# Kernel optimization log

Measured on AMD Instinct MI355X. Metric: run time of the kernel, lower is better.

The kernel has to match this reference:

```python
import jax, jax.numpy as jnp
import numpy as np

N_GRAPH = 10000
IN_DIM = 256
HID = 256
N_NODES = 16
FEAT_DIM = 64
N_EDGES = 5
TAU = 0.01


def _gat(x, src, dst, W, al, ar, R, b, H, D, N):
    # DGL GATConv: fc -> per-head attention logits -> edge softmax over dst -> aggregate, residual fc, bias
    h = (x @ W).reshape(N, H, D)                      # [N,H,D]
    el = jnp.sum(h * al[None], -1)                    # [N,H]
    er = jnp.sum(h * ar[None], -1)                    # [N,H]
    e = jax.nn.leaky_relu(el[src] + er[dst], 0.2)     # [E,H]
    m = jax.ops.segment_max(e, dst, num_segments=N)
    ex = jnp.exp(e - m[dst])
    s = jax.ops.segment_sum(ex, dst, num_segments=N)
    alpha = ex / s[dst]                               # [E,H]
    out = jax.ops.segment_sum(alpha[:, :, None] * h[src], dst, num_segments=N)  # [N,H,D]
    out = out + (x @ R).reshape(N, H, D) + b.reshape(1, H, D)
    return out.reshape(N, H * D)


def _masked_softmax(vec, mask, eps=1e-8):
    m = mask.astype(vec.dtype)
    _vec = vec * m - 10000.0 * (1.0 - m)
    vmax = jnp.max(_vec, axis=-1, keepdims=True)
    exps = jnp.exp((vec - vmax) * m) * m
    return exps / (jnp.sum(exps, -1, keepdims=True) + eps)


def _sample_edges(probs, target_idx):
    n, T = probs.shape
    mask = jnp.arange(T) == target_idx                # [T] bool, one-hot of target
    edges = [jnp.full((n,), target_idx, dtype=jnp.int32)]
    key = jax.random.key(42)
    for i in range(N_EDGES - 1):
        p = _masked_softmax(probs, jnp.logical_not(mask))
        idx = jax.random.categorical(jax.random.fold_in(key, i),
                                     jnp.log(jnp.maximum(p, 1e-30)), axis=-1)  # [n]
        mask = jnp.logical_or(jax.nn.one_hot(idx, T, dtype=bool), mask)
        edges.append(idx.astype(jnp.int32))
    return jnp.stack(edges, axis=-1)                  # [n, N_EDGES]


def _forward(feat, W1a, al1a, ar1a, R1a, b1a, W1e, al1e, ar1e, R1e, b1e,
             W2a, al2a, ar2a, R2a, b2a, W2e, al2e, ar2e, R2e, b2e,
             Wt, bt, Wo, bo, src, dst, target_idx):
    N = feat.shape[0]
    tf = jax.nn.leaky_relu(feat[target_idx] @ Wt + bt, 0.01)            # [2*HID]
    a = _gat(feat, src, dst, W1a, al1a, ar1a, R1a, b1a, 4, HID // 4, N)  # [N,HID]
    e = _gat(feat, src, dst, W1e, al1e, ar1e, R1e, b1e, 4, HID // 4, N)  # [N,HID]
    a2 = jax.nn.leaky_relu(jnp.concatenate([a, e], -1) + tf, 0.01)       # [N,2*HID]
    e2 = jax.nn.leaky_relu(jnp.concatenate([e, a], -1) + tf, 0.01)
    a3 = _gat(a2, src, dst, W2a, al2a, ar2a, R2a, b2a, 4, N_NODES * FEAT_DIM // 4, N)  # [N, n_nodes*feat_dim]
    e3 = _gat(e2, src, dst, W2e, al2e, ar2e, R2e, b2e, 1, N_NODES, N)                  # [N, n_nodes]
    attr = a3.reshape(N, N_NODES, FEAT_DIM).mean(0)                     # [n_nodes, feat_dim]
    node_attr = jax.nn.leaky_relu(attr, 0.01) @ Wo + bo                 # [n_nodes, input_dim]
    probs = jax.nn.softmax(e3.T, axis=-1)                               # [n_nodes, N]
    return node_attr, probs


def setup_inputs() -> dict:
    key = jax.random.key(0)
    ks = jax.random.split(key, 32)
    N, IN, H = N_GRAPH, IN_DIM, 4
    E0 = 80000
    feat = jax.random.normal(ks[0], (N, IN), jnp.float32)
    loop = jnp.arange(N, dtype=jnp.int32)
    src = jnp.concatenate([jax.random.randint(ks[1], (E0,), 0, N, jnp.int32), loop])
    dst = jnp.concatenate([jax.random.randint(ks[2], (E0,), 0, N, jnp.int32), loop])

    def p(k, shape, fan):
        return jax.random.normal(k, shape, jnp.float32) * (1.0 / np.sqrt(fan))

    D1 = HID // 4
    D2a = N_NODES * FEAT_DIM // 4
    O2a = N_NODES * FEAT_DIM
    inp = dict(feat=feat, src=src, dst=dst, target_idx=7)
    # layer-1 attr / edge GATs
    inp.update(W1a=p(ks[3], (IN, HID), IN), al1a=p(ks[4], (H, D1), D1), ar1a=p(ks[5], (H, D1), D1),
               R1a=p(ks[6], (IN, HID), IN), b1a=p(ks[7], (HID,), HID))
    inp.update(W1e=p(ks[8], (IN, HID), IN), al1e=p(ks[9], (H, D1), D1), ar1e=p(ks[10], (H, D1), D1),
               R1e=p(ks[11], (IN, HID), IN), b1e=p(ks[12], (HID,), HID))
    # layer-2 attr GAT (4 heads) and edge GAT (1 head)
    inp.update(W2a=p(ks[13], (2 * HID, O2a), 2 * HID), al2a=p(ks[14], (H, D2a), D2a), ar2a=p(ks[15], (H, D2a), D2a),
               R2a=p(ks[16], (2 * HID, O2a), 2 * HID), b2a=p(ks[17], (O2a,), O2a))
    inp.update(W2e=p(ks[18], (2 * HID, N_NODES), 2 * HID), al2e=p(ks[19], (1, N_NODES), N_NODES),
               ar2e=p(ks[20], (1, N_NODES), N_NODES), R2e=p(ks[21], (2 * HID, N_NODES), 2 * HID),
               b2e=p(ks[22], (N_NODES,), N_NODES))
    # target feat layer and attr output layer
    inp.update(Wt=p(ks[23], (IN, 2 * HID), IN), bt=p(ks[24], (2 * HID,), 2 * HID),
               Wo=p(ks[25], (FEAT_DIM, IN), FEAT_DIM), bo=p(ks[26], (IN,), IN))
    return inp


def reference(feat, W1a, al1a, ar1a, R1a, b1a, W1e, al1e, ar1e, R1e, b1e,
              W2a, al2a, ar2a, R2a, b2a, W2e, al2e, ar2e, R2e, b2e,
              Wt, bt, Wo, bo, src, dst, target_idx):
    node_attr, probs = _forward(feat, W1a, al1a, ar1a, R1a, b1a, W1e, al1e, ar1e, R1e, b1e,
                                W2a, al2a, ar2a, R2a, b2a, W2e, al2e, ar2e, R2e, b2e,
                                Wt, bt, Wo, bo, src, dst, target_idx)
    node_edges = _sample_edges(probs, target_idx)
    # (node_attr, attr_sample_weights, node_edges, normalized_edge_sample_weights)
    return node_attr, node_attr, node_edges, probs
```

## Files before the change

kernel.cpp:

```cpp
#include <hip/hip_runtime.h>
#include <hip/hip_bf16.h>

#define NGR 10000
typedef unsigned int u32;
typedef __attribute__((ext_vector_type(8))) short short8;
typedef __attribute__((ext_vector_type(4))) float f32x4;

__device__ __forceinline__ void threefry(u32 k0, u32 k1, u32 c0, u32 c1, u32& o0, u32& o1) {
    u32 ks2 = k0 ^ k1 ^ 0x1BD11BDAu;
    u32 x0 = c0 + k0, x1 = c1 + k1;
#define TF_R(r) { x0 += x1; x1 = (x1 << r) | (x1 >> (32 - r)); x1 ^= x0; }
    TF_R(13) TF_R(15) TF_R(26) TF_R(6)
    x0 += k1; x1 += ks2 + 1u;
    TF_R(17) TF_R(29) TF_R(16) TF_R(24)
    x0 += ks2; x1 += k0 + 2u;
    TF_R(13) TF_R(15) TF_R(26) TF_R(6)
    x0 += k0; x1 += k1 + 3u;
    TF_R(17) TF_R(29) TF_R(16) TF_R(24)
    x0 += k1; x1 += ks2 + 4u;
    TF_R(13) TF_R(15) TF_R(26) TF_R(6)
    x0 += ks2; x1 += k0 + 5u;
#undef TF_R
    o0 = x0; o1 = x1;
}

__global__ void k_deg(const int* __restrict__ dst, int* __restrict__ deg, int E) {
    int i = blockIdx.x * blockDim.x + threadIdx.x;
    if (i < E) atomicAdd(&deg[dst[i]], 1);
}
__global__ void k_scan(const int* __restrict__ deg, int* __restrict__ rowptr, int n) {
    __shared__ int sums[256];
    __shared__ int excl[257];
    const int T = 256;
    int t = threadIdx.x;
    int per = (n + T - 1) / T;
    int lo = t * per, hi = min(lo + per, n);
    int s = 0;
    for (int i = lo; i < hi; ++i) s += deg[i];
    sums[t] = s;
    __syncthreads();
    if (t == 0) { int run = 0; for (int i = 0; i < T; ++i) { excl[i] = run; run += sums[i]; } excl[T] = run; }
    __syncthreads();
    int run = excl[t];
    for (int i = lo; i < hi; ++i) { rowptr[i] = run; run += deg[i]; }
    if (t == 0) rowptr[n] = excl[T];
}
__global__ void k_scatter(const int* __restrict__ dst, const int* __restrict__ rowptr,
                          int* __restrict__ cursor, int* __restrict__ colidx, int E) {
    int i = blockIdx.x * blockDim.x + threadIdx.x;
    if (i >= E) return;
    int d = dst[i];
    int pos = atomicAdd(&cursor[d], 1);
    colidx[rowptr[d] + pos] = i;
}

#define TINYF 1.17549435e-38f
__global__ __launch_bounds__(256) void k_prep(
    const float* __restrict__ feat, const int* __restrict__ tptr,
    const float* __restrict__ Wt, const float* __restrict__ bt,
    const float* __restrict__ W1a, const float* __restrict__ W1e,
    const float* __restrict__ R1a, const float* __restrict__ R1e,
    const float* __restrict__ b1a, const float* __restrict__ b1e,
    const float* __restrict__ W2a, const float* __restrict__ al2a, const float* __restrict__ ar2a,
    unsigned short* __restrict__ feathi, unsigned short* __restrict__ featlo,
    unsigned short* __restrict__ WThi, unsigned short* __restrict__ WTlo,
    float* __restrict__ tf, float* __restrict__ gum, float* __restrict__ wal,
    float* __restrict__ packb, float* __restrict__ zreg)
{
    __shared__ float sh[32 * 33];
    int b = blockIdx.x, tid = threadIdx.x;
    if (b < 2500) {
        int idx = b * 256 + tid;
        float4 v = ((const float4*)feat)[idx];
        ushort4 h, l;
        __hip_bfloat16 bb; float r;
        bb = __float2bfloat16(v.x); h.x = *(unsigned short*)&bb; r = v.x - __bfloat162float(bb);
        bb = __float2bfloat16(r);   l.x = *(unsigned short*)&bb;
        bb = __float2bfloat16(v.y); h.y = *(unsigned short*)&bb; r = v.y - __bfloat162float(bb);
        bb = __float2bfloat16(r);   l.y = *(unsigned short*)&bb;
        bb = __float2bfloat16(v.z); h.z = *(unsigned short*)&bb; r = v.z - __bfloat162float(bb);
        bb = __float2bfloat16(r);   l.z = *(unsigned short*)&bb;
        bb = __float2bfloat16(v.w); h.w = *(unsigned short*)&bb; r = v.w - __bfloat162float(bb);
        bb = __float2bfloat16(r);   l.w = *(unsigned short*)&bb;
        ((ushort4*)feathi)[idx] = h;
        ((ushort4*)featlo)[idx] = l;
        return;
    }
    b -= 2500;
    if (b < 256) {
        int bx = b >> 3, by = b & 7;
        int tx = tid & 31, ty = tid >> 5;
#pragma unroll
        for (int i = ty; i < 32; i += 8) {
            int k = by * 32 + i, c = bx * 32 + tx;
            float v;
            if (c < 256) v = W1a[k * 256 + c];
            else if (c < 512) v = W1e[k * 256 + c - 256];
            else if (c < 768) v = R1a[k * 256 + c - 512];
            else v = R1e[k * 256 + c - 768];
            sh[i * 33 + tx] = v;
        }
        __syncthreads();
#pragma unroll
        for (int i = ty; i < 32; i += 8) {
            float x = sh[tx * 33 + i];
            __hip_bfloat16 bh = __float2bfloat16(x);
            float r = x - __bfloat162float(bh);
            __hip_bfloat16 bl = __float2bfloat16(r);
            WThi[(size_t)(bx * 32 + i) * 256 + by * 32 + tx] = *(unsigned short*)&bh;
            WTlo[(size_t)(bx * 32 + i) * 256 + by * 32 + tx] = *(unsigned short*)&bl;
        }
        return;
    }
    b -= 256;
    if (b < 8) {
        float* frow = sh;
        float* red = sh + 256;
        int t = *tptr;
        frow[tid] = feat[t * 256 + tid];
        __syncthreads();
        int j = b * 64 + (tid & 63);
        int ks = (tid >> 6) * 64;
        float s = 0.f;
#pragma unroll 16
        for (int k = ks; k < ks + 64; ++k) s = fmaf(frow[k], Wt[(size_t)k * 512 + j], s);
        red[tid] = s;
        __syncthreads();
        if (tid < 64) {
            float v = red[tid] + red[tid + 64] + red[tid + 128] + red[tid + 192] + bt[j];
            tf[j] = v >= 0.f ? v : 0.01f * v;
        }
        return;
    }
    b -= 8;
    if (b < 2500) {
        int idx = b * 256 + tid;
        int it = idx / (16 * NGR);
        int f = idx - it * (16 * NGR);
        u32 fk0, fk1, o0, o1;
        threefry(0u, 42u, 0u, (u32)it, fk0, fk1);
        threefry(fk0, fk1, 0u, (u32)f, o0, o1);
        u32 bits = o0 ^ o1;
        float fl = __uint_as_float((bits >> 9) | 0x3F800000u) - 1.0f;
        float u = fmaxf(TINYF, fl + TINYF);
        gum[idx] = -logf(-logf(u));
        return;
    }
    b -= 2500;
    if (b < 16) {
        int o = b * 256 + tid;
        int k = o >> 3, q = o & 7, sel = q >> 2, hh = q & 3;
        const float* av = (sel ? ar2a : al2a) + hh * 256;
        const float* wr = W2a + (size_t)k * 1024 + hh * 256;
        float s = 0.f;
        for (int d = 0; d < 256; ++d) s = fmaf(wr[d], av[d], s);
        wal[k * 8 + q] = s;
        return;
    }
    b -= 16;
    if (b < 235) {
        int idx = b * 256 + tid;
        if (idx < NGR * 6) zreg[idx] = 0.f;
        return;
    }
    b -= 235;
    {
        int c = b * 256 + tid;
        packb[c] = (c < 512) ? 0.f : ((c < 768) ? b1a[c - 512] : b1e[c - 768]);
    }
}

__global__ __launch_bounds__(256) void gemm_bf16x3(
    const unsigned short* __restrict__ Ahi, const unsigned short* __restrict__ Alo,
    const unsigned short* __restrict__ Bhi, const unsigned short* __restrict__ Blo,
    float* __restrict__ C, const float* __restrict__ bias, int M)
{
    constexpr int K = 256;
    __shared__ unsigned short AsH[2][128 * 32];
    __shared__ unsigned short AsL[2][128 * 32];
    __shared__ unsigned short BsH[2][128 * 32];
    __shared__ unsigned short BsL[2][128 * 32];
    const int tid = threadIdx.x;
    const int lane = tid & 63;
    const int w = tid >> 6, wr = w >> 1, wc = w & 1;
    const int bm = blockIdx.y * 128, bn = blockIdx.x * 128;
    const int fr = lane & 15, fq = lane >> 4;
    const int srow = tid >> 2;
    const int sbyte = (tid & 3) * 16;
    f32x4 acc[4][4] = {};

    auto stage = [&](int b, int k0) {
        const char* pA[2] = {(const char*)Ahi, (const char*)Alo};
        const char* pB[2] = {(const char*)Bhi, (const char*)Blo};
        char* dA[2] = {(char*)AsH[b], (char*)AsL[b]};
        char* dB[2] = {(char*)BsH[b], (char*)BsL[b]};
#pragma unroll
        for (int q = 0; q < 2; ++q) {
            const char* ga0 = pA[q] + ((size_t)(bm + srow) * K + k0) * 2 + sbyte;
            const char* ga1 = pA[q] + ((size_t)(bm + 64 + srow) * K + k0) * 2 + sbyte;
            const char* gb0 = pB[q] + ((size_t)(bn + srow) * K + k0) * 2 + sbyte;
            const char* gb1 = pB[q] + ((size_t)(bn + 64 + srow) * K + k0) * 2 + sbyte;
            __builtin_amdgcn_global_load_lds((const __attribute__((address_space(1))) void*)ga0,
                (__attribute__((address_space(3))) void*)(dA[q] + tid * 16), 16, 0, 0);
            __builtin_amdgcn_global_load_lds((const __attribute__((address_space(1))) void*)ga1,
                (__attribute__((address_space(3))) void*)(dA[q] + 4096 + tid * 16), 16, 0, 0);
            __builtin_amdgcn_global_load_lds((const __attribute__((address_space(1))) void*)gb0,
                (__attribute__((address_space(3))) void*)(dB[q] + tid * 16), 16, 0, 0);
            __builtin_amdgcn_global_load_lds((const __attribute__((address_space(1))) void*)gb1,
                (__attribute__((address_space(3))) void*)(dB[q] + 4096 + tid * 16), 16, 0, 0);
        }
    };

    stage(0, 0);
    __syncthreads();
    int buf = 0;
    for (int t = 0; t < 8; ++t) {
        if (t < 7) stage(buf ^ 1, (t + 1) * 32);
        const char* ah = (const char*)AsH[buf];
        const char* al = (const char*)AsL[buf];
        const char* bh = (const char*)BsH[buf];
        const char* bl = (const char*)BsL[buf];
        short8 afh[4], afl[4], bfh[4], bfl[4];
#pragma unroll
        for (int m = 0; m < 4; ++m) {
            int o = (wr * 64 + m * 16 + fr) * 64 + fq * 16;
            afh[m] = *(const short8*)(ah + o);
            afl[m] = *(const short8*)(al + o);
        }
#pragma unroll
        for (int n = 0; n < 4; ++n) {
            int o = (wc * 64 + n * 16 + fr) * 64 + fq * 16;
            bfh[n] = *(const short8*)(bh + o);
            bfl[n] = *(const short8*)(bl + o);
        }
#pragma unroll
        for (int m = 0; m < 4; ++m)
#pragma unroll
            for (int n = 0; n < 4; ++n) {
                acc[m][n] = __builtin_amdgcn_mfma_f32_16x16x32_bf16(afl[m], bfh[n], acc[m][n], 0, 0, 0);
                acc[m][n] = __builtin_amdgcn_mfma_f32_16x16x32_bf16(afh[m], bfl[n], acc[m][n], 0, 0, 0);
                acc[m][n] = __builtin_amdgcn_mfma_f32_16x16x32_bf16(afh[m], bfh[n], acc[m][n], 0, 0, 0);
            }
        __syncthreads();
        buf ^= 1;
    }
#pragma unroll
    for (int m = 0; m < 4; ++m) {
#pragma unroll
        for (int i = 0; i < 4; ++i) {
            int row = bm + wr * 64 + m * 16 + fq * 4 + i;
            if (row >= M) continue;
#pragma unroll
            for (int n = 0; n < 4; ++n) {
                int col = bn + wc * 64 + n * 16 + fr;
                C[(size_t)row * 1024 + col] = acc[m][n][i] + bias[col];
            }
        }
    }
}

__global__ void k_el_er_l1(const float* __restrict__ h,
                           const float* __restrict__ al1a, const float* __restrict__ ar1a,
                           const float* __restrict__ al1e, const float* __restrict__ ar1e,
                           float* __restrict__ el, float* __restrict__ er, int N)
{
    int idx = blockIdx.x * blockDim.x + threadIdx.x;
    if (idx >= N * 8) return;
    int n = idx >> 3, sub = idx & 7;
    int role = sub >> 2, hh = sub & 3;
    const float* hp = h + (size_t)n * 1024 + role * 256 + hh * 64;
    const float* alp = (role ? al1e : al1a) + hh * 64;
    const float* arp = (role ? ar1e : ar1a) + hh * 64;
    float sl = 0.f, sr = 0.f;
    for (int d = 0; d < 64; d += 4) {
        float4 v = *(const float4*)(hp + d);
        float4 a4 = *(const float4*)(alp + d);
        float4 r4 = *(const float4*)(arp + d);
        sl = fmaf(v.x, a4.x, sl); sl = fmaf(v.y, a4.y, sl); sl = fmaf(v.z, a4.z, sl); sl = fmaf(v.w, a4.w, sl);
        sr = fmaf(v.x, r4.x, sr); sr = fmaf(v.y, r4.y, sr); sr = fmaf(v.z, r4.z, sr); sr = fmaf(v.w, r4.w, sr);
    }
    el[n * 8 + sub] = sl;
    er[n * 8 + sub] = sr;
}

__global__ void k_softmax_csr(const float* __restrict__ el, const float* __restrict__ er,
                              const int* __restrict__ rowptr, const int* __restrict__ colidx,
                              const int* __restrict__ src,
                              float* __restrict__ ee, int H, int hshift, int total)
{
    int idx = blockIdx.x * blockDim.x + threadIdx.x;
    if (idx >= total) return;
    int n = idx >> hshift, hh = idx & (H - 1);
    float ern = er[n * H + hh];
    int i0 = rowptr[n], i1 = rowptr[n + 1];
    float mx = -INFINITY;
    for (int i = i0; i < i1; ++i) {
        float v = el[src[colidx[i]] * H + hh] + ern;
        v = v >= 0.f ? v : 0.2f * v;
        mx = fmaxf(mx, v);
    }
    float s = 0.f;
    for (int i = i0; i < i1; ++i) {
        int e = colidx[i];
        float v = el[src[e] * H + hh] + ern;
        v = v >= 0.f ? v : 0.2f * v;
        float ex = expf(v - mx);
        ee[(size_t)e * H + hh] = ex;
        s += ex;
    }
    for (int i = i0; i < i1; ++i) {
        int e = colidx[i];
        ee[(size_t)e * H + hh] /= s;
    }
}

__global__ void k_agg_csr4(const float* __restrict__ alpha,
                           const int* __restrict__ rowptr, const int* __restrict__ colidx,
                           const int* __restrict__ src,
                           const float* __restrict__ h, int ldh4, int hoff4,
                           float* __restrict__ out, int ldo4, int ooff4,
                           int H, int dshift4, int hdshift4, int total)
{
    int idx = blockIdx.x * blockDim.x + threadIdx.x;
    if (idx >= total) return;
    int n = idx >> hdshift4, c4 = idx & ((1 << hdshift4) - 1);
    int hh = c4 >> dshift4;
    const float4* h4 = (const float4*)h;
    float4* out4 = (float4*)out;
    float4 acc = out4[(size_t)n * ldo4 + ooff4 + c4];
    int i1 = rowptr[n + 1];
    for (int i = rowptr[n]; i < i1; ++i) {
        int e = colidx[i];
        float a = alpha[(size_t)e * H + hh];
        float4 hv = h4[(size_t)src[e] * ldh4 + hoff4 + c4];
        acc.x = fmaf(a, hv.x, acc.x); acc.y = fmaf(a, hv.y, acc.y);
        acc.z = fmaf(a, hv.z, acc.z); acc.w = fmaf(a, hv.w, acc.w);
    }
    out4[(size_t)n * ldo4 + ooff4 + c4] = acc;
}

__global__ void k_a2e2(const float* __restrict__ h1o1, const float* __restrict__ tf,
                       float* __restrict__ B)
{
    int idx = blockIdx.x * blockDim.x + threadIdx.x;
    if (idx >= NGR * 256) return;
    int n = idx >> 8, c4 = idx & 255;
    int c = c4 << 2;
    const float* o = h1o1 + (size_t)n * 1024 + 512;
    float4 x;
    if (c < 512) x = *(const float4*)(o + c);
    else { int cc = c - 512; x = *(const float4*)(o + ((cc < 256) ? cc + 256 : cc - 256)); }
    float4 t4 = *(const float4*)(tf + (c & 511));
    x.x += t4.x; x.y += t4.y; x.z += t4.z; x.w += t4.w;
    x.x = x.x >= 0.f ? x.x : 0.01f * x.x;
    x.y = x.y >= 0.f ? x.y : 0.01f * x.y;
    x.z = x.z >= 0.f ? x.z : 0.01f * x.z;
    x.w = x.w >= 0.f ? x.w : 0.01f * x.w;
    *(float4*)(B + (size_t)n * 1024 + c) = x;
}

__global__ __launch_bounds__(256) void k_node_linear(
    const float* __restrict__ a2e2,
    const float* __restrict__ We, const float* __restrict__ Re, const float* __restrict__ be,
    const float* __restrict__ wal,
    const float* __restrict__ al2e, const float* __restrict__ ar2e,
    float* __restrict__ h2e, float* __restrict__ e3,
    float* __restrict__ el2e, float* __restrict__ er2e,
    float* __restrict__ el2a, float* __restrict__ er2a)
{
    __shared__ float As[8 * 1024];
    __shared__ float red[2048];
    __shared__ float hl[8][16];
    int tid = threadIdx.x;
    int m0 = blockIdx.x * 8;
    for (int i = tid; i < 8 * 256; i += 256) {
        int row = i >> 8, c4 = (i & 255) << 2;
        *(float4*)(As + row * 1024 + c4) = *(const float4*)(a2e2 + (size_t)(m0 + row) * 1024 + c4);
    }
    __syncthreads();
    {
        int j = tid & 31, ks = tid >> 5;
        const float* B = (j < 16) ? We : Re;
        int jj = j & 15;
        float acc[8] = {};
        int k0 = ks * 64;
        for (int kk = 0; kk < 64; kk += 4) {
            int k = k0 + kk;
            float b0 = B[(k + 0) * 16 + jj];
            float b1 = B[(k + 1) * 16 + jj];
            float b2 = B[(k + 2) * 16 + jj];
            float b3 = B[(k + 3) * 16 + jj];
#pragma unroll
            for (int r = 0; r < 8; ++r) {
                float4 a = *(const float4*)(As + r * 1024 + 512 + k);
                acc[r] = fmaf(a.x, b0, acc[r]);
                acc[r] = fmaf(a.y, b1, acc[r]);
                acc[r] = fmaf(a.z, b2, acc[r]);
                acc[r] = fmaf(a.w, b3, acc[r]);
            }
        }
#pragma unroll
        for (int r = 0; r < 8; ++r) red[(r * 32 + j) * 8 + ks] = acc[r];
    }
    __syncthreads();
    {
        int r = tid >> 5, jo = tid & 31;
        const float* rp = red + (r * 32 + jo) * 8;
        float acc = ((rp[0] + rp[1]) + (rp[2] + rp[3])) + ((rp[4] + rp[5]) + (rp[6] + rp[7]));
        int m = m0 + r, jj = jo & 15;
        if (jo < 16) { h2e[(size_t)m * 16 + jj] = acc; hl[r][jj] = acc; }
        else         e3[(size_t)m * 16 + jj] = acc + be[jj];
    }
    __syncthreads();
    {
        int q = tid & 7, ks2 = tid >> 3;
        float acc[8] = {};
        int k0 = ks2 * 16;
        for (int kk = 0; kk < 16; ++kk) {
            int k = k0 + kk;
            float b = wal[k * 8 + q];
#pragma unroll
            for (int r = 0; r < 8; ++r)
                acc[r] = fmaf(As[r * 1024 + k], b, acc[r]);
        }
#pragma unroll
        for (int r = 0; r < 8; ++r) red[(r * 8 + q) * 32 + ks2] = acc[r];
    }
    __syncthreads();
    if (tid < 64) {
        const float* rp = red + tid * 32;
        float acc = 0.f;
#pragma unroll
        for (int g = 0; g < 32; ++g) acc += rp[g];
        int r = tid >> 3, q = tid & 7;
        int m = m0 + r;
        if (q < 4) el2a[m * 4 + q] = acc;
        else       er2a[m * 4 + (q - 4)] = acc;
    }
    if (tid >= 64 && tid < 72) {
        int rr = tid - 64;
        float sl = 0.f, sr = 0.f;
        const float* hp = hl[rr];
        for (int d = 0; d < 16; ++d) { float v = hp[d]; sl = fmaf(v, al2e[d], sl); sr = fmaf(v, ar2e[d], sr); }
        el2e[m0 + rr] = sl;
        er2e[m0 + rr] = sr;
    }
}

__global__ void k_sm2a_wa(const float* __restrict__ el, const float* __restrict__ er,
                          const int* __restrict__ rowptr, const int* __restrict__ colidx,
                          const int* __restrict__ src,
                          float* __restrict__ walpha, int total)
{
    int idx = blockIdx.x * blockDim.x + threadIdx.x;
    if (idx >= total) return;
    int n = idx >> 2, hh = idx & 3;
    float ern = er[n * 4 + hh];
    int i0 = rowptr[n], i1 = rowptr[n + 1];
    float mx = -INFINITY;
    for (int i = i0; i < i1; ++i) {
        float v = el[src[colidx[i]] * 4 + hh] + ern;
        v = v >= 0.f ? v : 0.2f * v;
        mx = fmaxf(mx, v);
    }
    float s = 0.f;
    for (int i = i0; i < i1; ++i) {
        float v = el[src[colidx[i]] * 4 + hh] + ern;
        v = v >= 0.f ? v : 0.2f * v;
        s += expf(v - mx);
    }
    for (int i = i0; i < i1; ++i) {
        int e = colidx[i];
        int sn = src[e];
        float v = el[sn * 4 + hh] + ern;
        v = v >= 0.f ? v : 0.2f * v;
        float alpha = expf(v - mx) / s;
        atomicAdd(&walpha[sn * 4 + hh], alpha);
    }
}

__global__ void k_smagg2e(const float* __restrict__ el, const float* __restrict__ er,
                          const int* __restrict__ rowptr, const int* __restrict__ colidx,
                          const int* __restrict__ src,
                          const float* __restrict__ h2e, float* __restrict__ e3, int N)
{
    int n = blockIdx.x * blockDim.x + threadIdx.x;
    if (n >= N) return;
    float ern = er[n];
    int i0 = rowptr[n], i1 = rowptr[n + 1];
    float mx = -INFINITY;
    for (int i = i0; i < i1; ++i) {
        float v = el[src[colidx[i]]] + ern;
        v = v >= 0.f ? v : 0.2f * v;
        mx = fmaxf(mx, v);
    }
    float s = 0.f;
    for (int i = i0; i < i1; ++i) {
        float v = el[src[colidx[i]]] + ern;
        v = v >= 0.f ? v : 0.2f * v;
        s += expf(v - mx);
    }
    float4* e34 = (float4*)(e3 + (size_t)n * 16);
    float4 a0 = e34[0], a1 = e34[1], a2 = e34[2], a3 = e34[3];
    for (int i = i0; i < i1; ++i) {
        int e = colidx[i];
        int sn = src[e];
        float v = el[sn] + ern;
        v = v >= 0.f ? v : 0.2f * v;
        float al = expf(v - mx) / s;
        const float4* hp = (const float4*)(h2e + (size_t)sn * 16);
        float4 h0 = hp[0], h1 = hp[1], h2 = hp[2], h3 = hp[3];
        a0.x = fmaf(al, h0.x, a0.x); a0.y = fmaf(al, h0.y, a0.y); a0.z = fmaf(al, h0.z, a0.z); a0.w = fmaf(al, h0.w, a0.w);
        a1.x = fmaf(al, h1.x, a1.x); a1.y = fmaf(al, h1.y, a1.y); a1.z = fmaf(al, h1.z, a1.z); a1.w = fmaf(al, h1.w, a1.w);
        a2.x = fmaf(al, h2.x, a2.x); a2.y = fmaf(al, h2.y, a2.y); a2.z = fmaf(al, h2.z, a2.z); a2.w = fmaf(al, h2.w, a2.w);
        a3.x = fmaf(al, h3.x, a3.x); a3.y = fmaf(al, h3.y, a3.y); a3.z = fmaf(al, h3.z, a3.z); a3.w = fmaf(al, h3.w, a3.w);
    }
    e34[0] = a0; e34[1] = a1; e34[2] = a2; e34[3] = a3;
}

__global__ __launch_bounds__(256) void k_pwa(const float* __restrict__ a2e2,
                                             const float* __restrict__ walpha,
                                             float* __restrict__ pwa)
{
    int b = blockIdx.x, t = threadIdx.x;
    float acc[5][2] = {};
    int n0 = b * 80, n1 = min(n0 + 80, NGR);
    for (int n = n0; n < n1; ++n) {
        const float* row = a2e2 + (size_t)n * 1024;
        const float* wa = walpha + n * 4;
        float w0 = wa[0], w1 = wa[1], w2 = wa[2], w3 = wa[3];
        float x0 = row[t], x1 = row[t + 256];
        acc[0][0] = fmaf(w0, x0, acc[0][0]); acc[0][1] = fmaf(w0, x1, acc[0][1]);
        acc[1][0] = fmaf(w1, x0, acc[1][0]); acc[1][1] = fmaf(w1, x1, acc[1][1]);
        acc[2][0] = fmaf(w2, x0, acc[2][0]); acc[2][1] = fmaf(w2, x1, acc[2][1]);
        acc[3][0] = fmaf(w3, x0, acc[3][0]); acc[3][1] = fmaf(w3, x1, acc[3][1]);
        acc[4][0] += x0; acc[4][1] += x1;
    }
#pragma unroll
    for (int q = 0; q < 5; ++q) {
        pwa[(size_t)b * 2560 + q * 512 + t] = acc[q][0];
        pwa[(size_t)b * 2560 + q * 512 + t + 256] = acc[q][1];
    }
}
__global__ void k_pwa_fin(const float* __restrict__ pwa, float* __restrict__ waw)
{
    int idx = blockIdx.x * blockDim.x + threadIdx.x;
    if (idx >= 2560) return;
    float s = 0.f;
    for (int b = 0; b < 125; ++b) s += pwa[(size_t)b * 2560 + idx];
    waw[idx] = s;
}

__global__ __launch_bounds__(256) void k_gemv3(const float* __restrict__ waw,
                                               const float* __restrict__ W2a, const float* __restrict__ R2a,
                                               const float* __restrict__ b2a,
                                               float* __restrict__ attrL)
{
    __shared__ float red[256];
    int b = blockIdx.x, t = threadIdx.x;
    int c = b * 16 + (t & 15);
    int hh = (b * 16) >> 8;
    int ks = (t >> 4) * 32;
    const float* wh = waw + hh * 512;
    const float* w4 = waw + 4 * 512;
    float s = 0.f;
#pragma unroll 8
    for (int k = ks; k < ks + 32; ++k) {
        s = fmaf(wh[k], W2a[(size_t)k * 1024 + c], s);
        s = fmaf(w4[k], R2a[(size_t)k * 1024 + c], s);
    }
    red[t] = s;
    __syncthreads();
    if (t < 16) {
        float v = 0.f;
#pragma unroll
        for (int g = 0; g < 16; ++g) v += red[t + g * 16];
        v = v / (float)NGR + b2a[b * 16 + t];
        attrL[b * 16 + t] = v >= 0.f ? v : 0.01f * v;
    }
}

__global__ __launch_bounds__(256) void k_nattr2(const float* __restrict__ attrL,
                                                const float* __restrict__ Wo, const float* __restrict__ bo,
                                                float* __restrict__ out)
{
    __shared__ float al[64];
    int i = blockIdx.x, t = threadIdx.x;
    if (t < 64) al[t] = attrL[i * 64 + t];
    __syncthreads();
    float acc = 0.f;
#pragma unroll 8
    for (int d = 0; d < 64; ++d) acc = fmaf(al[d], Wo[d * 256 + t], acc);
    acc += bo[t];
    out[i * 256 + t] = acc;
    out[4096 + i * 256 + t] = acc;
}

__global__ __launch_bounds__(256) void k_e3stats(const float* __restrict__ e3,
                                                 float* __restrict__ pm, float* __restrict__ ps)
{
    __shared__ float lds[4000];
    __shared__ float redm[16][16];
    __shared__ float reds[16][16];
    __shared__ float cm[16];
    int b = blockIdx.x, tid = threadIdx.x;
    int base = b * 250 * 16;
    for (int i = tid; i < 4000; i += 256) lds[i] = e3[base + i];
    __syncthreads();
    int c = tid & 15, g = tid >> 4;
    float mx = -INFINITY;
    for (int q = g; q < 250; q += 16) mx = fmaxf(mx, lds[q * 16 + c]);
    redm[c][g] = mx;
    __syncthreads();
    if (tid < 16) {
        float m = redm[tid][0];
        for (int q = 1; q < 16; ++q) m = fmaxf(m, redm[tid][q]);
        cm[tid] = m;
    }
    __syncthreads();
    float mb = cm[c];
    float s = 0.f;
    for (int q = g; q < 250; q += 16) s += expf(lds[q * 16 + c] - mb);
    reds[c][g] = s;
    __syncthreads();
    if (tid < 16) {
        float ss = 0.f;
        for (int q = 0; q < 16; ++q) ss += reds[tid][q];
        pm[b * 16 + tid] = cm[tid];
        ps[b * 16 + tid] = ss;
    }
}
__global__ void k_e3fin(const float* __restrict__ pm, const float* __restrict__ ps,
                        float* __restrict__ mx16, float* __restrict__ ss16)
{
    int c = threadIdx.x;
    if (c >= 16) return;
    float M = -INFINITY;
    for (int b = 0; b < 40; ++b) M = fmaxf(M, pm[b * 16 + c]);
    float S = 0.f;
    for (int b = 0; b < 40; ++b) S += ps[b * 16 + c] * expf(pm[b * 16 + c] - M);
    mx16[c] = M;
    ss16[c] = S;
}

__global__ __launch_bounds__(256) void k_top5(const float* __restrict__ e3, const float* __restrict__ gum,
                                              const float* __restrict__ mx16, const float* __restrict__ ss16,
                                              float* __restrict__ probs,
                                              float* __restrict__ t5v, int* __restrict__ t5i)
{
    __shared__ float wv[4];
    __shared__ int wi[4];
    int chunk = blockIdx.x, y = blockIdx.y;
    int it = y >> 4, r = y & 15;
    int tid = threadIdx.x, lane = tid & 63, wid = tid >> 6;
    float mxr = mx16[r], ssr = ss16[r];
    const float* g = gum + (size_t)y * NGR;
    int jb = chunk * 1250;
    float sv[5]; int si[5];
#pragma unroll
    for (int q = 0; q < 5; ++q) {
        int o = q * 256 + tid;
        float s = -INFINITY; int idx = 0x7FFFFFFF;
        if (o < 1250) {
            int j = jb + o;
            float p = expf(e3[(size_t)j * 16 + r] - mxr) / ssr;
            if (it == 0) probs[(size_t)r * NGR + j] = p;
            s = g[j] + p;
            idx = j;
        }
        sv[q] = s; si[q] = idx;
    }
    int outb = (y * 8 + chunk) * 5;
    for (int round = 0; round < 5; ++round) {
        float best = sv[0]; int bi = si[0];
#pragma unroll
        for (int q = 1; q < 5; ++q)
            if (sv[q] > best || (sv[q] == best && si[q] < bi)) { best = sv[q]; bi = si[q]; }
#pragma unroll
        for (int o = 32; o > 0; o >>= 1) {
            float ov = __shfl_xor(best, o, 64); int oi = __shfl_xor(bi, o, 64);
            if (ov > best || (ov == best && oi < bi)) { best = ov; bi = oi; }
        }
        if (lane == 0) { wv[wid] = best; wi[wid] = bi; }
        __syncthreads();
        float gbv = wv[0]; int gbi = wi[0];
#pragma unroll
        for (int w2 = 1; w2 < 4; ++w2) {
            float ov = wv[w2]; int oi = wi[w2];
            if (ov > gbv || (ov == gbv && oi < gbi)) { gbv = ov; gbi = oi; }
        }
        if (tid == 0) { t5v[outb + round] = gbv; t5i[outb + round] = gbi; }
#pragma unroll
        for (int q = 0; q < 5; ++q) if (si[q] == gbi) { sv[q] = -INFINITY; si[q] = 0x7FFFFFFF; }
        __syncthreads();
    }
}

__global__ void k_select(const int* __restrict__ tptr, const float* __restrict__ t5v,
                         const int* __restrict__ t5i, float* __restrict__ out_edges)
{
    int r = threadIdx.x;
    if (r >= 16) return;
    int s0 = *tptr, s1 = -1, s2 = -1, s3 = -1;
    out_edges[r * 5] = (float)s0;
    for (int it = 0; it < 4; ++it) {
        float best = -INFINITY; int bi = 0x7FFFFFFF;
        int base = (it * 16 + r) * 40;
        for (int c = 0; c < 40; ++c) {
            int idx = t5i[base + c];
            if (idx == s0 || idx == s1 || idx == s2 || idx == s3) continue;
            float v = t5v[base + c];
            if (v > best || (v == best && idx < bi)) { best = v; bi = idx; }
        }
        if (it == 0) s1 = bi; else if (it == 1) s2 = bi; else if (it == 2) s3 = bi;
        out_edges[r * 5 + it + 1] = (float)bi;
    }
}

extern "C" void kernel_launch(void* const* d_in, const int* in_sizes, int n_in,
                              void* d_out, int out_size, void* d_ws, size_t ws_size,
                              hipStream_t stream)
{
    const float* feat = (const float*)d_in[0];
    const int* src = (const int*)d_in[1];
    const int* dst = (const int*)d_in[2];
    const int* tptr = (const int*)d_in[3];
    const float* W1a = (const float*)d_in[4];  const float* al1a = (const float*)d_in[5];
    const float* ar1a = (const float*)d_in[6]; const float* R1a = (const float*)d_in[7];
    const float* b1a = (const float*)d_in[8];
    const float* W1e = (const float*)d_in[9];  const float* al1e = (const float*)d_in[10];
    const float* ar1e = (const float*)d_in[11]; const float* R1e = (const float*)d_in[12];
    const float* b1e = (const float*)d_in[13];
    const float* W2a = (const float*)d_in[14]; const float* al2a = (const float*)d_in[15];
    const float* ar2a = (const float*)d_in[16]; const float* R2a = (const float*)d_in[17];
    const float* b2a = (const float*)d_in[18];
    const float* W2e = (const float*)d_in[19]; const float* al2e = (const float*)d_in[20];
    const float* ar2e = (const float*)d_in[21]; const float* R2e = (const float*)d_in[22];
    const float* b2e = (const float*)d_in[23];
    const float* Wt = (const float*)d_in[24];  const float* bt = (const float*)d_in[25];
    const float* Wo = (const float*)d_in[26];  const float* bo = (const float*)d_in[27];
    const int E = in_sizes[1];
    const int N = NGR;

    float* ws = (float*)d_ws;
    float* regionA = ws;
    size_t off = (size_t)N * 1024;
    auto alloc = [&](size_t n) { float* p = ws + off; off += (n + 3) & ~(size_t)3; return p; };
    float* a2e2 = alloc((size_t)N * 1024);
    float* tf   = alloc(512);
    float* el1  = alloc((size_t)N * 8);
    float* er1  = alloc((size_t)N * 8);
    float* el2a = alloc((size_t)N * 4);
    float* er2a = alloc((size_t)N * 4);
    float* el2e = alloc(N);
    float* er2e = alloc(N);
    float* h2e  = alloc((size_t)N * 16);
    float* e3   = alloc((size_t)N * 16);
    float* ee1  = alloc((size_t)E * 8);
    float* packb = alloc(1024);
    float* gum   = alloc((size_t)4 * 16 * NGR);
    float* wal   = alloc(512 * 8);
    float* pwa   = alloc(125 * 2560);
    float* waw   = alloc(2560);
    float* attrL = alloc(1024);
    float* pm    = alloc(40 * 16);
    float* ps    = alloc(40 * 16);
    float* mx16  = alloc(16);
    float* ss16  = alloc(16);
    float* t5v   = alloc(64 * 40);
    int*   t5i   = (int*)alloc(64 * 40);
    unsigned short* feathi = (unsigned short*)alloc((size_t)10112 * 128);
    unsigned short* featlo = (unsigned short*)alloc((size_t)10112 * 128);
    unsigned short* WThi = (unsigned short*)alloc((size_t)1024 * 128);
    unsigned short* WTlo = (unsigned short*)alloc((size_t)1024 * 128);
    float* zstart = alloc((size_t)N * 6);
    float* walpha = zstart;
    int* deg    = (int*)(zstart + (size_t)N * 4);
    int* cursor = deg + N;
    int* rowptr = (int*)alloc(N + 1);
    int* colidx = (int*)alloc(E);

    float* out = (float*)d_out;
    float* out_edges = out + 8192;
    float* out_probs = out + 8272;

    dim3 blk(256);

    k_prep<<<5519, blk, 0, stream>>>(feat, tptr, Wt, bt, W1a, W1e, R1a, R1e, b1a, b1e,
                                     W2a, al2a, ar2a, feathi, featlo, WThi, WTlo,
                                     tf, gum, wal, packb, zstart);
    k_deg<<<(E + 255) / 256, blk, 0, stream>>>(dst, deg, E);
    k_scan<<<1, blk, 0, stream>>>(deg, rowptr, N);
    k_scatter<<<(E + 255) / 256, blk, 0, stream>>>(dst, rowptr, cursor, colidx, E);

    gemm_bf16x3<<<dim3(8, 79), blk, 0, stream>>>(feathi, featlo, WThi, WTlo, regionA, packb, N);
    k_el_er_l1<<<(N * 8 + 255) / 256, blk, 0, stream>>>(regionA, al1a, ar1a, al1e, ar1e, el1, er1, N);
    k_softmax_csr<<<(N * 8 + 255) / 256, blk, 0, stream>>>(el1, er1, rowptr, colidx, src, ee1, 8, 3, N * 8);
    k_agg_csr4<<<(N * 128 + 255) / 256, blk, 0, stream>>>(ee1, rowptr, colidx, src,
                                                          regionA, 256, 0, regionA, 256, 128,
                                                          8, 4, 7, N * 128);
    k_a2e2<<<(N * 256 + 255) / 256, blk, 0, stream>>>(regionA, tf, a2e2);

    k_node_linear<<<N / 8, blk, 0, stream>>>(a2e2, W2e, R2e, b2e, wal, al2e, ar2e,
                                             h2e, e3, el2e, er2e, el2a, er2a);
    k_sm2a_wa<<<(N * 4 + 255) / 256, blk, 0, stream>>>(el2a, er2a, rowptr, colidx, src, walpha, N * 4);
    k_smagg2e<<<(N + 255) / 256, blk, 0, stream>>>(el2e, er2e, rowptr, colidx, src, h2e, e3, N);

    k_pwa<<<125, blk, 0, stream>>>(a2e2, walpha, pwa);
    k_pwa_fin<<<10, blk, 0, stream>>>(pwa, waw);
    k_gemv3<<<64, blk, 0, stream>>>(waw, W2a, R2a, b2a, attrL);
    k_nattr2<<<16, blk, 0, stream>>>(attrL, Wo, bo, out);

    k_e3stats<<<40, blk, 0, stream>>>(e3, pm, ps);
    k_e3fin<<<1, 64, 0, stream>>>(pm, ps, mx16, ss16);
    k_top5<<<dim3(8, 64), blk, 0, stream>>>(e3, gum, mx16, ss16, out_probs, t5v, t5i);
    k_select<<<1, 64, 0, stream>>>(tptr, t5v, t5i, out_edges);
}
```

Before: 361.4 us.

## Fuse small GAT stages to cut kernel launches and intermediate buffers

Several adjacent kernels are merged. The layer-1 aggregation now writes the leaky-relu'd a2e2 tensor directly instead of round-tripping through regionA. The two layer-2 softmax kernels become one launch. The pwa reduction, gemv and node-attr output are combined into a single 16-block kernel, and the e3 final-stats step is folded into top5. This is meant to remove launch overhead and global memory traffic for intermediates. In exchange, the fused attr kernel runs on only 16 blocks and recomputes the column sums redundantly in each block, and every top5 block repeats the 40-entry stats reduction.

```diff
diff --git a/kernel.cpp b/kernel.cpp
--- a/kernel.cpp
+++ b/kernel.cpp
@@ -314,49 +314,43 @@
     }
 }
 
-__global__ void k_agg_csr4(const float* __restrict__ alpha,
+__global__ void k_agg_a2e2(const float* __restrict__ alpha,
                            const int* __restrict__ rowptr, const int* __restrict__ colidx,
                            const int* __restrict__ src,
-                           const float* __restrict__ h, int ldh4, int hoff4,
-                           float* __restrict__ out, int ldo4, int ooff4,
-                           int H, int dshift4, int hdshift4, int total)
+                           const float* __restrict__ regionA, const float* __restrict__ tf,
+                           float* __restrict__ a2e2, int total)
 {
     int idx = blockIdx.x * blockDim.x + threadIdx.x;
     if (idx >= total) return;
-    int n = idx >> hdshift4, c4 = idx & ((1 << hdshift4) - 1);
-    int hh = c4 >> dshift4;
-    const float4* h4 = (const float4*)h;
-    float4* out4 = (float4*)out;
-    float4 acc = out4[(size_t)n * ldo4 + ooff4 + c4];
+    int n = idx >> 7, c4 = idx & 127;
+    int hh = c4 >> 4;
+    const float4* h4 = (const float4*)regionA;
+    float4 acc = h4[(size_t)n * 256 + 128 + c4];
     int i1 = rowptr[n + 1];
     for (int i = rowptr[n]; i < i1; ++i) {
         int e = colidx[i];
-        float a = alpha[(size_t)e * H + hh];
-        float4 hv = h4[(size_t)src[e] * ldh4 + hoff4 + c4];
+        float a = alpha[(size_t)e * 8 + hh];
+        float4 hv = h4[(size_t)src[e] * 256 + c4];
         acc.x = fmaf(a, hv.x, acc.x); acc.y = fmaf(a, hv.y, acc.y);
         acc.z = fmaf(a, hv.z, acc.z); acc.w = fmaf(a, hv.w, acc.w);
     }
-    out4[(size_t)n * ldo4 + ooff4 + c4] = acc;
-}
-
-__global__ void k_a2e2(const float* __restrict__ h1o1, const float* __restrict__ tf,
-                       float* __restrict__ B)
-{
-    int idx = blockIdx.x * blockDim.x + threadIdx.x;
-    if (idx >= NGR * 256) return;
-    int n = idx >> 8, c4 = idx & 255;
     int c = c4 << 2;
-    const float* o = h1o1 + (size_t)n * 1024 + 512;
-    float4 x;
-    if (c < 512) x = *(const float4*)(o + c);
-    else { int cc = c - 512; x = *(const float4*)(o + ((cc < 256) ? cc + 256 : cc - 256)); }
-    float4 t4 = *(const float4*)(tf + (c & 511));
-    x.x += t4.x; x.y += t4.y; x.z += t4.z; x.w += t4.w;
-    x.x = x.x >= 0.f ? x.x : 0.01f * x.x;
-    x.y = x.y >= 0.f ? x.y : 0.01f * x.y;
-    x.z = x.z >= 0.f ? x.z : 0.01f * x.z;
-    x.w = x.w >= 0.f ? x.w : 0.01f * x.w;
-    *(float4*)(B + (size_t)n * 1024 + c) = x;
+    int cc = (c + 256) & 511;
+    float4 ta = *(const float4*)(tf + c);
+    float4 te = *(const float4*)(tf + cc);
+    float4 xa, xe;
+    xa.x = acc.x + ta.x; xa.y = acc.y + ta.y; xa.z = acc.z + ta.z; xa.w = acc.w + ta.w;
+    xe.x = acc.x + te.x; xe.y = acc.y + te.y; xe.z = acc.z + te.z; xe.w = acc.w + te.w;
+    xa.x = xa.x >= 0.f ? xa.x : 0.01f * xa.x;
+    xa.y = xa.y >= 0.f ? xa.y : 0.01f * xa.y;
+    xa.z = xa.z >= 0.f ? xa.z : 0.01f * xa.z;
+    xa.w = xa.w >= 0.f ? xa.w : 0.01f * xa.w;
+    xe.x = xe.x >= 0.f ? xe.x : 0.01f * xe.x;
+    xe.y = xe.y >= 0.f ? xe.y : 0.01f * xe.y;
+    xe.z = xe.z >= 0.f ? xe.z : 0.01f * xe.z;
+    xe.w = xe.w >= 0.f ? xe.w : 0.01f * xe.w;
+    *(float4*)(a2e2 + (size_t)n * 1024 + c) = xa;
+    *(float4*)(a2e2 + (size_t)n * 1024 + 512 + cc) = xe;
 }
 
 __global__ __launch_bounds__(256) void k_node_linear(
@@ -447,56 +441,53 @@
     }
 }
 
-__global__ void k_sm2a_wa(const float* __restrict__ el, const float* __restrict__ er,
-                          const int* __restrict__ rowptr, const int* __restrict__ colidx,
-                          const int* __restrict__ src,
-                          float* __restrict__ walpha, int total)
+__global__ void k_sm_l2(const float* __restrict__ el2a, const float* __restrict__ er2a,
+                        const float* __restrict__ el2e, const float* __restrict__ er2e,
+                        const int* __restrict__ rowptr, const int* __restrict__ colidx,
+                        const int* __restrict__ src,
+                        const float* __restrict__ h2e,
+                        float* __restrict__ walpha, float* __restrict__ e3, int N)
 {
     int idx = blockIdx.x * blockDim.x + threadIdx.x;
-    if (idx >= total) return;
-    int n = idx >> 2, hh = idx & 3;
-    float ern = er[n * 4 + hh];
+    if (idx < N * 4) {
+        int n = idx >> 2, hh = idx & 3;
+        float ern = er2a[n * 4 + hh];
+        int i0 = rowptr[n], i1 = rowptr[n + 1];
+        float mx = -INFINITY;
+        for (int i = i0; i < i1; ++i) {
+            float v = el2a[src[colidx[i]] * 4 + hh] + ern;
+            v = v >= 0.f ? v : 0.2f * v;
+            mx = fmaxf(mx, v);
+        }
+        float s = 0.f;
+        for (int i = i0; i < i1; ++i) {
+            float v = el2a[src[colidx[i]] * 4 + hh] + ern;
+            v = v >= 0.f ? v : 0.2f * v;
+            s += expf(v - mx);
+        }
+        for (int i = i0; i < i1; ++i) {
+            int e = colidx[i];
+            int sn = src[e];
+            float v = el2a[sn * 4 + hh] + ern;
+            v = v >= 0.f ? v : 0.2f * v;
+            float alpha = expf(v - mx) / s;
+            atomicAdd(&walpha[sn * 4 + hh], alpha);
+        }
+        return;
+    }
+    int n = idx - N * 4;
+    if (n >= N) return;
+    float ern = er2e[n];
     int i0 = rowptr[n], i1 = rowptr[n + 1];
     float mx = -INFINITY;
     for (int i = i0; i < i1; ++i) {
-        float v = el[src[colidx[i]] * 4 + hh] + ern;
+        float v = el2e[src[colidx[i]]] + ern;
         v = v >= 0.f ? v : 0.2f * v;
         mx = fmaxf(mx, v);
     }
     float s = 0.f;
     for (int i = i0; i < i1; ++i) {
-        float v = el[src[colidx[i]] * 4 + hh] + ern;
-        v = v >= 0.f ? v : 0.2f * v;
-        s += expf(v - mx);
-    }
-    for (int i = i0; i < i1; ++i) {
-        int e = colidx[i];
-        int sn = src[e];
-        float v = el[sn * 4 + hh] + ern;
-        v = v >= 0.f ? v : 0.2f * v;
-        float alpha = expf(v - mx) / s;
-        atomicAdd(&walpha[sn * 4 + hh], alpha);
-    }
-}
-
-__global__ void k_smagg2e(const float* __restrict__ el, const float* __restrict__ er,
-                          const int* __restrict__ rowptr, const int* __restrict__ colidx,
-                          const int* __restrict__ src,
-                          const float* __restrict__ h2e, float* __restrict__ e3, int N)
-{
-    int n = blockIdx.x * blockDim.x + threadIdx.x;
-    if (n >= N) return;
-    float ern = er[n];
-    int i0 = rowptr[n], i1 = rowptr[n + 1];
-    float mx = -INFINITY;
-    for (int i = i0; i < i1; ++i) {
-        float v = el[src[colidx[i]]] + ern;
-        v = v >= 0.f ? v : 0.2f * v;
-        mx = fmaxf(mx, v);
-    }
-    float s = 0.f;
-    for (int i = i0; i < i1; ++i) {
-        float v = el[src[colidx[i]]] + ern;
+        float v = el2e[src[colidx[i]]] + ern;
         v = v >= 0.f ? v : 0.2f * v;
         s += expf(v - mx);
     }
@@ -505,7 +496,7 @@
     for (int i = i0; i < i1; ++i) {
         int e = colidx[i];
         int sn = src[e];
-        float v = el[sn] + ern;
+        float v = el2e[sn] + ern;
         v = v >= 0.f ? v : 0.2f * v;
         float al = expf(v - mx) / s;
         const float4* hp = (const float4*)(h2e + (size_t)sn * 16);
@@ -542,55 +533,46 @@
         pwa[(size_t)b * 2560 + q * 512 + t + 256] = acc[q][1];
     }
 }
-__global__ void k_pwa_fin(const float* __restrict__ pwa, float* __restrict__ waw)
-{
-    int idx = blockIdx.x * blockDim.x + threadIdx.x;
-    if (idx >= 2560) return;
+
+__global__ __launch_bounds__(256) void k_attr_all(const float* __restrict__ pwa,
+                                                  const float* __restrict__ W2a, const float* __restrict__ R2a,
+                                                  const float* __restrict__ b2a,
+                                                  const float* __restrict__ Wo, const float* __restrict__ bo,
+                                                  float* __restrict__ out)
+{
+    __shared__ float whS[512];
+    __shared__ float w4S[512];
+    __shared__ float red[256];
+    __shared__ float attrLS[64];
+    int i = blockIdx.x, t = threadIdx.x;
+    int hh = i >> 2;
+#pragma unroll
+    for (int u = 0; u < 4; ++u) {
+        int g = u * 256 + t;
+        int col = (g < 512) ? (hh * 512 + g) : (4 * 512 + (g - 512));
+        float s = 0.f;
+        for (int b = 0; b < 125; ++b) s += pwa[(size_t)b * 2560 + col];
+        if (g < 512) whS[g] = s; else w4S[g - 512] = s;
+    }
+    __syncthreads();
+    int d = t & 63, ks = t >> 6;
+    int c = i * 64 + d;
     float s = 0.f;
-    for (int b = 0; b < 125; ++b) s += pwa[(size_t)b * 2560 + idx];
-    waw[idx] = s;
-}
-
-__global__ __launch_bounds__(256) void k_gemv3(const float* __restrict__ waw,
-                                               const float* __restrict__ W2a, const float* __restrict__ R2a,
-                                               const float* __restrict__ b2a,
-                                               float* __restrict__ attrL)
-{
-    __shared__ float red[256];
-    int b = blockIdx.x, t = threadIdx.x;
-    int c = b * 16 + (t & 15);
-    int hh = (b * 16) >> 8;
-    int ks = (t >> 4) * 32;
-    const float* wh = waw + hh * 512;
-    const float* w4 = waw + 4 * 512;
-    float s = 0.f;
-#pragma unroll 8
-    for (int k = ks; k < ks + 32; ++k) {
-        s = fmaf(wh[k], W2a[(size_t)k * 1024 + c], s);
-        s = fmaf(w4[k], R2a[(size_t)k * 1024 + c], s);
+    for (int k = ks * 128; k < ks * 128 + 128; ++k) {
+        s = fmaf(whS[k], W2a[(size_t)k * 1024 + c], s);
+        s = fmaf(w4S[k], R2a[(size_t)k * 1024 + c], s);
     }
     red[t] = s;
     __syncthreads();
-    if (t < 16) {
-        float v = 0.f;
-#pragma unroll
-        for (int g = 0; g < 16; ++g) v += red[t + g * 16];
-        v = v / (float)NGR + b2a[b * 16 + t];
-        attrL[b * 16 + t] = v >= 0.f ? v : 0.01f * v;
-    }
-}
-
-__global__ __launch_bounds__(256) void k_nattr2(const float* __restrict__ attrL,
-                                                const float* __restrict__ Wo, const float* __restrict__ bo,
-                                                float* __restrict__ out)
-{
-    __shared__ float al[64];
-    int i = blockIdx.x, t = threadIdx.x;
-    if (t < 64) al[t] = attrL[i * 64 + t];
+    if (t < 64) {
+        float v = red[t] + red[t + 64] + red[t + 128] + red[t + 192];
+        v = v / (float)NGR + b2a[c];
+        attrLS[t] = v >= 0.f ? v : 0.01f * v;
+    }
     __syncthreads();
     float acc = 0.f;
 #pragma unroll 8
-    for (int d = 0; d < 64; ++d) acc = fmaf(al[d], Wo[d * 256 + t], acc);
+    for (int dd = 0; dd < 64; ++dd) acc = fmaf(attrLS[dd], Wo[dd * 256 + t], acc);
     acc += bo[t];
     out[i * 256 + t] = acc;
     out[4096 + i * 256 + t] = acc;
@@ -630,21 +612,9 @@
         ps[b * 16 + tid] = ss;
     }
 }
-__global__ void k_e3fin(const float* __restrict__ pm, const float* __restrict__ ps,
-                        float* __restrict__ mx16, float* __restrict__ ss16)
-{
-    int c = threadIdx.x;
-    if (c >= 16) return;
-    float M = -INFINITY;
-    for (int b = 0; b < 40; ++b) M = fmaxf(M, pm[b * 16 + c]);
-    float S = 0.f;
-    for (int b = 0; b < 40; ++b) S += ps[b * 16 + c] * expf(pm[b * 16 + c] - M);
-    mx16[c] = M;
-    ss16[c] = S;
-}
 
 __global__ __launch_bounds__(256) void k_top5(const float* __restrict__ e3, const float* __restrict__ gum,
-                                              const float* __restrict__ mx16, const float* __restrict__ ss16,
+                                              const float* __restrict__ pm, const float* __restrict__ ps,
                                               float* __restrict__ probs,
                                               float* __restrict__ t5v, int* __restrict__ t5i)
 {
@@ -653,7 +623,11 @@
     int chunk = blockIdx.x, y = blockIdx.y;
     int it = y >> 4, r = y & 15;
     int tid = threadIdx.x, lane = tid & 63, wid = tid >> 6;
-    float mxr = mx16[r], ssr = ss16[r];
+    float M = -INFINITY;
+    for (int b = 0; b < 40; ++b) M = fmaxf(M, pm[b * 16 + r]);
+    float S = 0.f;
+    for (int b = 0; b < 40; ++b) S += ps[b * 16 + r] * expf(pm[b * 16 + r] - M);
+    float mxr = M, ssr = S;
     const float* g = gum + (size_t)y * NGR;
     int jb = chunk * 1250;
     float sv[5]; int si[5];
@@ -761,12 +735,8 @@
     float* gum   = alloc((size_t)4 * 16 * NGR);
     float* wal   = alloc(512 * 8);
     float* pwa   = alloc(125 * 2560);
-    float* waw   = alloc(2560);
-    float* attrL = alloc(1024);
     float* pm    = alloc(40 * 16);
     float* ps    = alloc(40 * 16);
-    float* mx16  = alloc(16);
-    float* ss16  = alloc(16);
     float* t5v   = alloc(64 * 40);
     int*   t5i   = (int*)alloc(64 * 40);
     unsigned short* feathi = (unsigned short*)alloc((size_t)10112 * 128);
@@ -796,23 +766,18 @@
     gemm_bf16x3<<<dim3(8, 79), blk, 0, stream>>>(feathi, featlo, WThi, WTlo, regionA, packb, N);
     k_el_er_l1<<<(N * 8 + 255) / 256, blk, 0, stream>>>(regionA, al1a, ar1a, al1e, ar1e, el1, er1, N);
     k_softmax_csr<<<(N * 8 + 255) / 256, blk, 0, stream>>>(el1, er1, rowptr, colidx, src, ee1, 8, 3, N * 8);
-    k_agg_csr4<<<(N * 128 + 255) / 256, blk, 0, stream>>>(ee1, rowptr, colidx, src,
-                                                          regionA, 256, 0, regionA, 256, 128,
-                                                          8, 4, 7, N * 128);
-    k_a2e2<<<(N * 256 + 255) / 256, blk, 0, stream>>>(regionA, tf, a2e2);
+    k_agg_a2e2<<<(N * 128 + 255) / 256, blk, 0, stream>>>(ee1, rowptr, colidx, src,
+                                                          regionA, tf, a2e2, N * 128);
 
     k_node_linear<<<N / 8, blk, 0, stream>>>(a2e2, W2e, R2e, b2e, wal, al2e, ar2e,
                                              h2e, e3, el2e, er2e, el2a, er2a);
-    k_sm2a_wa<<<(N * 4 + 255) / 256, blk, 0, stream>>>(el2a, er2a, rowptr, colidx, src, walpha, N * 4);
-    k_smagg2e<<<(N + 255) / 256, blk, 0, stream>>>(el2e, er2e, rowptr, colidx, src, h2e, e3, N);
+    k_sm_l2<<<(N * 5 + 255) / 256, blk, 0, stream>>>(el2a, er2a, el2e, er2e,
+                                                     rowptr, colidx, src, h2e, walpha, e3, N);
 
     k_pwa<<<125, blk, 0, stream>>>(a2e2, walpha, pwa);
-    k_pwa_fin<<<10, blk, 0, stream>>>(pwa, waw);
-    k_gemv3<<<64, blk, 0, stream>>>(waw, W2a, R2a, b2a, attrL);
-    k_nattr2<<<16, blk, 0, stream>>>(attrL, Wo, bo, out);
+    k_attr_all<<<16, blk, 0, stream>>>(pwa, W2a, R2a, b2a, Wo, bo, out);
 
     k_e3stats<<<40, blk, 0, stream>>>(e3, pm, ps);
-    k_e3fin<<<1, 64, 0, stream>>>(pm, ps, mx16, ss16);
-    k_top5<<<dim3(8, 64), blk, 0, stream>>>(e3, gum, mx16, ss16, out_probs, t5v, t5i);
+    k_top5<<<dim3(8, 64), blk, 0, stream>>>(e3, gum, pm, ps, out_probs, t5v, t5i);
     k_select<<<1, 64, 0, stream>>>(tptr, t5v, t5i, out_edges);
 }
```

Result: slower. 379.0 us (+4.9%).
